# Kernel optimization log

Measured on AMD Instinct MI355X. Metric: run time of the kernel, lower is better.

## Reference

```python
import math
import jax, jax.numpy as jnp
import numpy as np

LOW_FREQ = 1
FACTOR = 1


def setup_inputs() -> dict:
    key = jax.random.key(0)
    x = jax.random.normal(key, (16, 4096, 256), dtype=jnp.float32)
    return {"x": x}


def reference(x):
    b, t, d = x.shape
    x_freq = jnp.fft.rfft(x, axis=1)  # (b, t//2+1, d) complex
    if t % 2 == 0:
        x_freq = x_freq[:, LOW_FREQ:-1]
        f = jnp.fft.rfftfreq(t)[LOW_FREQ:-1]
    else:
        x_freq = x_freq[:, LOW_FREQ:]
        f = jnp.fft.rfftfreq(t)[LOW_FREQ:]
    f = f.astype(jnp.float32)
    F = x_freq.shape[1]
    top_k = int(FACTOR * math.log(F))  # static (shape-derived)

    # top-k by magnitude along freq axis, independently per (b, d)
    xf_bdf = jnp.moveaxis(x_freq, 1, 2)              # (b, d, F)
    _, idx = jax.lax.top_k(jnp.abs(xf_bdf), top_k)   # (b, d, k) int32
    xf_sel = jnp.take_along_axis(xf_bdf, idx, axis=2)  # (b, d, k)
    xf_sel = jnp.moveaxis(xf_sel, 2, 1)              # (b, k, d)
    f_sel = jnp.moveaxis(f[idx], 2, 1)[:, :, None, :]  # (b, k, 1, d)

    # extrapolate: conj-pair frequencies, synthesize cosines, reduce over freq
    xf2 = jnp.concatenate([xf_sel, jnp.conj(xf_sel)], axis=1)  # (b, 2k, d)
    f2 = jnp.concatenate([f_sel, -f_sel], axis=1)              # (b, 2k, 1, d)
    tt = jnp.arange(t, dtype=jnp.float32)[None, None, :, None]  # (1,1,t,1)
    amp = (jnp.abs(xf2) * 2.0 / t)[:, :, None, :]   # (b, 2k, 1, d)
    phase = jnp.angle(xf2)[:, :, None, :]           # (b, 2k, 1, d)
    x_time = amp * jnp.cos(2.0 * math.pi * f2 * tt + phase)  # (b, 2k, t, d)
    return x_time.sum(axis=1)  # (b, t, d)
```

## Files before the change

### kernel.cpp

```cpp
#include <hip/hip_runtime.h>
#include <math.h>

#define T_LEN 4096
#define N2    2048
#define TOPK  7
#define NCH   256
#define R8F 0.70710678f

#define AD(a) ((a) + ((a) >> 3) + ((a) >> 8))

typedef float nt_f4 __attribute__((ext_vector_type(4)));

typedef float2 c32;
__device__ __forceinline__ c32 cadd(c32 a, c32 b) { return make_float2(a.x + b.x, a.y + b.y); }
__device__ __forceinline__ c32 csub(c32 a, c32 b) { return make_float2(a.x - b.x, a.y - b.y); }
__device__ __forceinline__ c32 cmul(c32 a, c32 w) {
    return make_float2(w.x * a.x - w.y * a.y, w.x * a.y + w.y * a.x);
}
__device__ __forceinline__ c32 csq(c32 a) {
    return make_float2(a.x * a.x - a.y * a.y, 2.0f * a.x * a.y);
}
__device__ __forceinline__ c32 mulnegi(c32 a) { return make_float2(a.y, -a.x); }

__global__ __launch_bounds__(256) void prep_kernel(
    const float* __restrict__ x, float* __restrict__ xt,
    double2* __restrict__ tw, float2* __restrict__ twf)
{
    if (blockIdx.x < 16) {
        int p = blockIdx.x * 256 + threadIdx.x;
        double th = -2.0 * 3.14159265358979323846 * (double)p / (double)T_LEN;
        double c = cos(th), s = sin(th);
        tw[p]  = make_double2(c, s);
        twf[p] = make_float2((float)c, (float)s);
        return;
    }
    __shared__ float tile[64][65];
    const int bid = blockIdx.x - 16;
    const int t0  = (bid & 63) * 64;
    const int c0  = ((bid >> 6) & 3) * 64;
    const int b   = bid >> 8;
    const int tx4 = (threadIdx.x & 15) * 4;
    const int ty  = threadIdx.x >> 4;

    const float* src = x + (size_t)b * T_LEN * NCH;
    for (int r = 0; r < 4; ++r) {
        int t = ty + r * 16;
        nt_f4 v = __builtin_nontemporal_load(
            (const nt_f4*)(src + (size_t)(t0 + t) * NCH + c0 + tx4));
        tile[t][tx4 + 0] = v.x; tile[t][tx4 + 1] = v.y;
        tile[t][tx4 + 2] = v.z; tile[t][tx4 + 3] = v.w;
    }
    __syncthreads();
    float* dst = xt + (size_t)b * NCH * T_LEN;
    for (int r = 0; r < 4; ++r) {
        int c = ty + r * 16;
        float4 v = make_float4(tile[tx4 + 0][c], tile[tx4 + 1][c],
                               tile[tx4 + 2][c], tile[tx4 + 3][c]);
        *(float4*)(dst + (size_t)(c0 + c) * T_LEN + t0 + tx4) = v;
    }
}

__device__ __forceinline__ void dft8_pw(c32 x[8], c32 w1)
{
    c32 t0 = cadd(x[0], x[4]), t4 = csub(x[0], x[4]);
    c32 t1 = cadd(x[1], x[5]), t5 = csub(x[1], x[5]);
    c32 t2 = cadd(x[2], x[6]), t6 = csub(x[2], x[6]);
    c32 t3 = cadd(x[3], x[7]), t7 = csub(x[3], x[7]);
    c32 s0 = cadd(t0, t2), s2 = csub(t0, t2);
    c32 s1 = cadd(t1, t3), s3 = csub(t1, t3);
    x[0] = cadd(s0, s1);
    x[4] = csub(s0, s1);
    c32 s3n = mulnegi(s3);
    x[2] = cadd(s2, s3n);
    x[6] = csub(s2, s3n);
    c32 c1 = make_float2(R8F * (t5.x + t5.y), R8F * (t5.y - t5.x));
    c32 c2 = mulnegi(t6);
    c32 c3 = make_float2(R8F * (t7.y - t7.x), -R8F * (t7.x + t7.y));
    c32 d0 = cadd(t4, c2), d1 = csub(t4, c2);
    c32 d2 = cadd(c1, c3), d3 = csub(c1, c3);
    x[1] = cadd(d0, d2);
    x[5] = csub(d0, d2);
    c32 d3n = mulnegi(d3);
    x[3] = cadd(d1, d3n);
    x[7] = csub(d1, d3n);

    c32 w2 = csq(w1);
    c32 w3 = cmul(w1, w2);
    c32 w4 = csq(w2);
    c32 w5 = cmul(w3, w2);
    c32 w6 = csq(w3);
    c32 w7 = cmul(w4, w3);
    x[1] = cmul(x[1], w1);
    x[2] = cmul(x[2], w2);
    x[3] = cmul(x[3], w3);
    x[4] = cmul(x[4], w4);
    x[5] = cmul(x[5], w5);
    x[6] = cmul(x[6], w6);
    x[7] = cmul(x[7], w7);
}

__device__ __forceinline__ unsigned long long packkey32(float mag, int k) {
    return ((unsigned long long)__float_as_uint(mag) << 32)
         | (unsigned long long)(2047 - k);
}

#define CSWAP(i, j) { unsigned long long a_ = keys[i], b_ = keys[j]; \
                      keys[i] = a_ > b_ ? a_ : b_; keys[j] = a_ > b_ ? b_ : a_; }

__global__ __launch_bounds__(256, 8) void fft_topk_kernel(
    const float* __restrict__ xt, const double2* __restrict__ tw,
    const float2* __restrict__ twf,
    int* __restrict__ k_out, float4* __restrict__ ab4)
{
    __shared__ float2 zz[AD(N2 - 1) + 3];
    __shared__ unsigned long long wavetop[4 * TOPK];
    __shared__ unsigned long long selkey[TOPK];

    const int tid = threadIdx.x;
    const int bc  = blockIdx.x;
    const float2* xcol2 = (const float2*)(xt + (size_t)bc * T_LEN);

    c32 x[8];
#pragma unroll
    for (int u = 0; u < 8; ++u)
        x[u] = xcol2[tid + (u << 8)];
    dft8_pw(x, twf[2 * tid]);
#pragma unroll
    for (int m = 0; m < 8; ++m)
        zz[AD((m << 8) + tid)] = x[m];
    __syncthreads();

    {
        const int g = tid >> 5, j2 = tid & 31, base = (g << 8) + j2;
#pragma unroll
        for (int u = 0; u < 8; ++u)
            x[u] = zz[AD(base + (u << 5))];
        dft8_pw(x, twf[16 * j2]);
#pragma unroll
        for (int m = 0; m < 8; ++m)
            zz[AD(base + (m << 5))] = x[m];
    }
    __syncthreads();

    {
        const int g3 = tid >> 2, j3 = tid & 3, base = (g3 << 5) + j3;
#pragma unroll
        for (int u = 0; u < 8; ++u)
            x[u] = zz[AD(base + (u << 2))];
        dft8_pw(x, twf[128 * j3]);
#pragma unroll
        for (int m = 0; m < 8; ++m)
            zz[AD(base + (m << 2))] = x[m];
    }
    __syncthreads();

#pragma unroll
    for (int q = 0; q < 2; ++q) {
        int h4 = ((q << 8) + tid) << 2;
#pragma unroll
        for (int r = 0; r < 4; ++r)
            x[q * 4 + r] = zz[AD(h4 + r)];
    }
    __syncthreads();
#pragma unroll
    for (int q = 0; q < 2; ++q) {
        c32 b0 = x[q*4+0], b1 = x[q*4+1], b2 = x[q*4+2], b3 = x[q*4+3];
        c32 e0 = cadd(b0, b2), e1 = csub(b0, b2);
        c32 e2 = cadd(b1, b3), e3 = csub(b1, b3);
        c32 e3n = mulnegi(e3);
        int kbase = ((tid & 7) << 6) | (((tid >> 3) & 7) << 3) | (q << 2) | (tid >> 6);
        zz[AD(kbase)]        = cadd(e0, e2);
        zz[AD(kbase + 1024)] = csub(e0, e2);
        zz[AD(kbase +  512)] = cadd(e1, e3n);
        zz[AD(kbase + 1536)] = csub(e1, e3n);
    }
    __syncthreads();

    unsigned long long keys[8];
#pragma unroll
    for (int j = 0; j < 4; ++j) {
        int k  = 1 + tid + (j << 8);
        int kp = N2 - k;
        float2 yk = zz[AD(k)];
        float2 yp = zz[AD(kp)];
        float Ar = 0.5f * (yk.x + yp.x), Ai = 0.5f * (yk.y - yp.y);
        float Br = 0.5f * (yk.y + yp.y), Bi = -0.5f * (yk.x - yp.x);
        float2 t = twf[k];
        float Cr = t.x * Br - t.y * Bi;
        float Ci = t.x * Bi + t.y * Br;
        float m1 = (Ar + Cr) * (Ar + Cr) + (Ai + Ci) * (Ai + Ci);
        float m2 = (Ar - Cr) * (Ar - Cr) + (Ai - Ci) * (Ai - Ci);
        keys[2 * j]     = packkey32(m1, k);
        keys[2 * j + 1] = (kp != k) ? packkey32(m2, kp) : 0ULL;
    }

    CSWAP(0,1) CSWAP(2,3) CSWAP(4,5) CSWAP(6,7)
    CSWAP(0,2) CSWAP(1,3) CSWAP(4,6) CSWAP(5,7)
    CSWAP(1,2) CSWAP(5,6)
    CSWAP(0,4) CSWAP(1,5) CSWAP(2,6) CSWAP(3,7)
    CSWAP(2,4) CSWAP(3,5)
    CSWAP(1,2) CSWAP(3,4) CSWAP(5,6)

    const int wv = tid >> 6, ln = tid & 63;
    unsigned long long lb = keys[0];

    for (int it = 0; it < TOPK; ++it) {
        unsigned int hl = (unsigned int)(lb >> 32);
        unsigned int h  = hl;
#pragma unroll
        for (int off = 32; off; off >>= 1) {
            unsigned int o = __shfl_xor(h, off);
            h = (o > h) ? o : h;
        }
        unsigned long long mask = __ballot(hl == h);
        unsigned long long v;
        if (__popcll(mask) == 1) {
            int src = __ffsll((long long)mask) - 1;
            v = ((unsigned long long)h << 32)
              | (unsigned long long)__shfl((unsigned int)lb, src);
        } else {
            unsigned int l = (hl == h) ? (unsigned int)lb : 0u;
#pragma unroll
            for (int off = 32; off; off >>= 1) {
                unsigned int o = __shfl_xor(l, off);
                l = (o > l) ? o : l;
            }
            v = ((unsigned long long)h << 32) | l;
        }
        if (ln == 0) wavetop[wv * TOPK + it] = v;
        if (v == lb && v) {
            keys[0]=keys[1]; keys[1]=keys[2]; keys[2]=keys[3]; keys[3]=keys[4];
            keys[4]=keys[5]; keys[5]=keys[6]; keys[6]=keys[7]; keys[7]=0ULL;
            lb = keys[0];
        }
    }
    __syncthreads();

    if (tid < 32) {
        unsigned long long v = (tid < 4 * TOPK) ? wavetop[tid] : 0ULL;
        for (int it = 0; it < TOPK; ++it) {
            unsigned long long m = v;
#pragma unroll
            for (int off = 16; off; off >>= 1) {
                unsigned long long o = __shfl_xor(m, off);
                if (o > m) m = o;
            }
            if (tid == 0) selkey[it] = m;
            if (m == v) v = 0ULL;
        }
    }
    __syncthreads();

    if (tid < TOPK) {
        int k  = 2047 - (int)(selkey[tid] & 2047ULL);
        float2 ykf = zz[AD(k)];
        float2 ypf = zz[AD(N2 - k)];
        double ykx = (double)ykf.x, yky = (double)ykf.y;
        double ypx = (double)ypf.x, ypy = (double)ypf.y;
        double Ar = 0.5 * (ykx + ypx), Ai = 0.5 * (yky - ypy);
        double Br = 0.5 * (yky + ypy), Bi = -0.5 * (ykx - ypx);
        double2 t = tw[k];
        double Xr = Ar + t.x * Br - t.y * Bi;
        double Xi = Ai + t.x * Bi + t.y * Br;
        k_out[tid * 4096 + bc] = k;
        ab4[tid * 4096 + bc] = make_float4(
            (float)( 4.0 * Xr / (double)T_LEN),
            (float)(-4.0 * Xi / (double)T_LEN),
            (float)t.x, (float)(-t.y));
    }
}

__global__ __launch_bounds__(256) void recon_kernel(
    const int* __restrict__ k_in, const float4* __restrict__ ab4,
    float* __restrict__ out)
{
    __shared__ float tile[16][256];

    const int tid   = threadIdx.x;
    const int chunk = blockIdx.x & 127;
    const int b     = blockIdx.x >> 7;
    const int bc    = (b << 8) + tid;
    const int n0    = chunk << 5;

    const float c0 = 6.28318530717958647692f / 4096.0f;
    float aa[TOPK], bb[TOPK];
    c32 z[TOPK], w[TOPK];
#pragma unroll
    for (int j = 0; j < TOPK; ++j) {
        int k    = k_in[j * 4096 + bc];
        float4 v = ab4[j * 4096 + bc];
        aa[j] = v.x; bb[j] = v.y; w[j] = make_float2(v.z, v.w);
        int m0 = (k * n0) & (T_LEN - 1);
        float ang = (float)m0 * c0;
        __sincosf(ang, &z[j].y, &z[j].x);
    }

    float* obase = out + ((size_t)b * T_LEN + n0) * NCH;
    for (int r = 0; r < 2; ++r) {
#pragma unroll
        for (int i = 0; i < 16; ++i) {
            float acc = 0.f;
#pragma unroll
            for (int j = 0; j < TOPK; ++j) {
                acc += aa[j] * z[j].x + bb[j] * z[j].y;
                z[j] = cmul(z[j], w[j]);
            }
            tile[i][tid] = acc;
        }
        __syncthreads();
#pragma unroll
        for (int s = 0; s < 4; ++s) {
            int fid = tid + (s << 8);
            int ni  = fid >> 6;
            int c4  = (fid & 63) << 2;
            nt_f4 v = { tile[ni][c4], tile[ni][c4 + 1],
                        tile[ni][c4 + 2], tile[ni][c4 + 3] };
            __builtin_nontemporal_store(v,
                (nt_f4*)(obase + (size_t)((r << 4) + ni) * NCH + c4));
        }
        __syncthreads();
    }
}

extern "C" void kernel_launch(void* const* d_in, const int* in_sizes, int n_in,
                              void* d_out, int out_size, void* d_ws, size_t ws_size,
                              hipStream_t stream) {
    const float* x   = (const float*)d_in[0];
    float*       out = (float*)d_out;
    char*        ws  = (char*)d_ws;

    double2* tw    = (double2*)(ws);
    int*     k_ws  = (int*)   (ws + 65536);
    float4*  ab_ws = (float4*)(ws + 180224);
    float2*  twf   = (float2*)(ws + 638976);

    prep_kernel     <<<16 + 4096, 256, 0, stream>>>(x, out, tw, twf);
    fft_topk_kernel <<<4096, 256, 0, stream>>>(out, tw, twf, k_ws, ab_ws);
    recon_kernel    <<<2048, 256, 0, stream>>>(k_ws, ab_ws, out);
}
```

Measured before the change: 172.7 us.

## Fuse first radix-8 FFT stage into the transpose prep kernel

The prep kernel now loads tiles of the input, applies a swizzled shared-memory layout, and performs the first radix-8 butterfly with twiddles before writing to global memory. The FFT kernel skips its first stage and reads these partially transformed columns straight from global memory. This removes one LDS round trip and barrier from the FFT kernel and halves the prep grid size, at the cost of per-thread double-precision cos/sin in prep and strided global reads in the FFT's second stage.

```diff
diff --git a/kernel.cpp b/kernel.cpp
--- a/kernel.cpp
+++ b/kernel.cpp
@@ -21,44 +21,6 @@
     return make_float2(a.x * a.x - a.y * a.y, 2.0f * a.x * a.y);
 }
 __device__ __forceinline__ c32 mulnegi(c32 a) { return make_float2(a.y, -a.x); }
-
-__global__ __launch_bounds__(256) void prep_kernel(
-    const float* __restrict__ x, float* __restrict__ xt,
-    double2* __restrict__ tw, float2* __restrict__ twf)
-{
-    if (blockIdx.x < 16) {
-        int p = blockIdx.x * 256 + threadIdx.x;
-        double th = -2.0 * 3.14159265358979323846 * (double)p / (double)T_LEN;
-        double c = cos(th), s = sin(th);
-        tw[p]  = make_double2(c, s);
-        twf[p] = make_float2((float)c, (float)s);
-        return;
-    }
-    __shared__ float tile[64][65];
-    const int bid = blockIdx.x - 16;
-    const int t0  = (bid & 63) * 64;
-    const int c0  = ((bid >> 6) & 3) * 64;
-    const int b   = bid >> 8;
-    const int tx4 = (threadIdx.x & 15) * 4;
-    const int ty  = threadIdx.x >> 4;
-
-    const float* src = x + (size_t)b * T_LEN * NCH;
-    for (int r = 0; r < 4; ++r) {
-        int t = ty + r * 16;
-        nt_f4 v = __builtin_nontemporal_load(
-            (const nt_f4*)(src + (size_t)(t0 + t) * NCH + c0 + tx4));
-        tile[t][tx4 + 0] = v.x; tile[t][tx4 + 1] = v.y;
-        tile[t][tx4 + 2] = v.z; tile[t][tx4 + 3] = v.w;
-    }
-    __syncthreads();
-    float* dst = xt + (size_t)b * NCH * T_LEN;
-    for (int r = 0; r < 4; ++r) {
-        int c = ty + r * 16;
-        float4 v = make_float4(tile[tx4 + 0][c], tile[tx4 + 1][c],
-                               tile[tx4 + 2][c], tile[tx4 + 3][c]);
-        *(float4*)(dst + (size_t)(c0 + c) * T_LEN + t0 + tx4) = v;
-    }
-}
 
 __device__ __forceinline__ void dft8_pw(c32 x[8], c32 w1)
 {
@@ -99,6 +61,64 @@
     x[7] = cmul(x[7], w7);
 }
 
+__global__ __launch_bounds__(256) void prep_kernel(
+    const float* __restrict__ x, float2* __restrict__ gz,
+    double2* __restrict__ tw, float2* __restrict__ twf)
+{
+    if (blockIdx.x < 16) {
+        int p = blockIdx.x * 256 + threadIdx.x;
+        double th = -2.0 * 3.14159265358979323846 * (double)p / (double)T_LEN;
+        double c = cos(th), s = sin(th);
+        tw[p]  = make_double2(c, s);
+        twf[p] = make_float2((float)c, (float)s);
+        return;
+    }
+    __shared__ float tile[256][32];
+    const int bid = blockIdx.x - 16;
+    const int jt = bid & 15;
+    const int ct = (bid >> 4) & 7;
+    const int b  = bid >> 7;
+    const int j0 = jt << 4, c0 = ct << 5;
+    const int tid = threadIdx.x;
+
+    const float* src = x + (size_t)b * T_LEN * NCH + c0;
+#pragma unroll
+    for (int s = 0; s < 8; ++s) {
+        int fid = tid + (s << 8);
+        int lr  = fid >> 3;
+        int qc  = (fid & 7) << 2;
+        int t   = (j0 << 1) + ((lr >> 5) << 9) + (lr & 31);
+        nt_f4 v = __builtin_nontemporal_load(
+            (const nt_f4*)(src + (size_t)t * NCH + qc));
+        int sc = qc ^ ((((lr & 7) ^ ((lr >> 3) & 7))) << 2);
+        *(nt_f4*)&tile[lr][sc] = v;
+    }
+    __syncthreads();
+
+    const int dj = tid & 15;
+    const int j  = j0 + dj;
+    double th = -3.14159265358979323846 * (double)j / 1024.0;
+    c32 w1 = make_float2((float)cos(th), (float)sin(th));
+
+    for (int h = 0; h < 2; ++h) {
+        const int cc = (tid >> 4) + (h << 4);
+        c32 xx[8];
+#pragma unroll
+        for (int u = 0; u < 8; ++u) {
+            int lr0 = (u << 5) + (dj << 1);
+            int lr1 = lr0 + 1;
+            int s0  = cc ^ ((((lr0 & 7) ^ ((lr0 >> 3) & 7))) << 2);
+            int s1  = cc ^ ((((lr1 & 7) ^ ((lr1 >> 3) & 7))) << 2);
+            xx[u] = make_float2(tile[lr0][s0], tile[lr1][s1]);
+        }
+        dft8_pw(xx, w1);
+        float2* gcol = gz + ((size_t)((b << 8) + c0 + cc)) * N2;
+#pragma unroll
+        for (int m = 0; m < 8; ++m)
+            gcol[(m << 8) + j] = xx[m];
+    }
+}
+
 __device__ __forceinline__ unsigned long long packkey32(float mag, int k) {
     return ((unsigned long long)__float_as_uint(mag) << 32)
          | (unsigned long long)(2047 - k);
@@ -118,23 +138,14 @@
 
     const int tid = threadIdx.x;
     const int bc  = blockIdx.x;
-    const float2* xcol2 = (const float2*)(xt + (size_t)bc * T_LEN);
+    const float2* gcol = ((const float2*)xt) + (size_t)bc * N2;
 
     c32 x[8];
-#pragma unroll
-    for (int u = 0; u < 8; ++u)
-        x[u] = xcol2[tid + (u << 8)];
-    dft8_pw(x, twf[2 * tid]);
-#pragma unroll
-    for (int m = 0; m < 8; ++m)
-        zz[AD((m << 8) + tid)] = x[m];
-    __syncthreads();
-
     {
         const int g = tid >> 5, j2 = tid & 31, base = (g << 8) + j2;
 #pragma unroll
         for (int u = 0; u < 8; ++u)
-            x[u] = zz[AD(base + (u << 5))];
+            x[u] = gcol[base + (u << 5)];
         dft8_pw(x, twf[16 * j2]);
 #pragma unroll
         for (int m = 0; m < 8; ++m)
@@ -334,7 +345,7 @@
     float4*  ab_ws = (float4*)(ws + 180224);
     float2*  twf   = (float2*)(ws + 638976);
 
-    prep_kernel     <<<16 + 4096, 256, 0, stream>>>(x, out, tw, twf);
+    prep_kernel     <<<16 + 2048, 256, 0, stream>>>(x, (float2*)out, tw, twf);
     fft_topk_kernel <<<4096, 256, 0, stream>>>(out, tw, twf, k_ws, ab_ws);
     recon_kernel    <<<2048, 256, 0, stream>>>(k_ws, ab_ws, out);
 }
```

After: 174.7 us. About the same (+1.2%).
